# Kernel optimization log

Measured on AMD Instinct MI355X. Metric: run time of the kernel, lower is better.

The kernel has to match this reference:

```python
import jax, jax.numpy as jnp
import numpy as np

L2_IDX = np.array([0, 1, 2, 4, 24, 26, 35, 38])
S = 16    # n_scalar_features
H = 32    # hidden multiplicity
NL2 = 9   # number of 2e inputs (8 selected kernels + kernel sum)
B = 131072
NK = 40   # n_kernels


def _w3j_222():
    """Wigner 3j / CG tensor for 2e x 2e -> 2e in the real spherical-harmonic
    basis, Frobenius-normalized (e3nn convention up to an overall sign).
    Computed as the 1-D null space of the infinitesimal equivariance constraint."""
    l = 2
    mv = np.arange(-l, l + 1)
    Jp = np.zeros((5, 5), complex)
    for i, m in enumerate(mv[:-1]):
        Jp[i + 1, i] = np.sqrt(l * (l + 1) - m * (m + 1))
    Jm = Jp.conj().T
    Jx, Jy, Jz = (Jp + Jm) / 2, (Jp - Jm) / 2j, np.diag(mv).astype(complex)
    # complex -> real spherical harmonics change of basis
    Q = np.zeros((5, 5), complex)
    for m in mv:
        i = m + l
        if m < 0:
            Q[i, i] = 1j / np.sqrt(2)
            Q[i, l - m] = -1j * (-1.0) ** m / np.sqrt(2)
        elif m == 0:
            Q[i, i] = 1.0
        else:
            Q[i, l - m] = 1 / np.sqrt(2)
            Q[i, i] = (-1.0) ** m / np.sqrt(2)
    Gs = [np.real(-1j * Q @ J @ Q.conj().T) for J in (Jx, Jy, Jz)]  # real so(3) generators
    I5, I25 = np.eye(5), np.eye(25)
    M = np.concatenate([np.kron(G, I25) + np.kron(I5, np.kron(G, I5)) + np.kron(I25, G)
                        for G in Gs], axis=0)
    c = np.linalg.svd(M)[2][-1].reshape(5, 5, 5)
    c = c / np.linalg.norm(c)
    if c.flat[np.argmax(np.abs(c))] < 0:
        c = -c
    return c.astype(np.float32)


C222 = jnp.asarray(_w3j_222())
INV_SQRT5 = float(1.0 / np.sqrt(5.0))  # CG value for l,l->0 and 0,l->l paths


def setup_inputs() -> dict:
    key = jax.random.key(0)
    ks = jax.random.split(key, 10)
    return {
        "scalars": jax.random.normal(ks[0], (B, S), jnp.float32),
        "kernel_t2s": jax.random.normal(ks[1], (B, NK, 5), jnp.float32),
        "w000": jax.random.normal(ks[2], (S, S, H), jnp.float32),
        "w110": jax.random.normal(ks[3], (NL2, NL2, H), jnp.float32),
        "w011": jax.random.normal(ks[4], (S, NL2, H), jnp.float32),
        "w101": jax.random.normal(ks[5], (NL2, S, H), jnp.float32),
        "w111": jax.random.normal(ks[6], (NL2, NL2, H), jnp.float32),
        "v010": jax.random.normal(ks[7], (H, H), jnp.float32),
        "v100": jax.random.normal(ks[8], (H, H), jnp.float32),
        "v110": jax.random.normal(ks[9], (H, H), jnp.float32),
    }


def reference(scalars, kernel_t2s, w000, w110, w011, w101, w111, v010, v100, v110):
    s = scalars                                                  # (B, S)   0e inputs
    t = jnp.concatenate([kernel_t2s[:, L2_IDX, :],
                         kernel_t2s.sum(axis=1, keepdims=True)], axis=1)  # (B, 9, 5) 2e inputs

    # e3nn path-normalization coefficients (component / element defaults)
    c0 = (1.0 / (S * S + NL2 * NL2 * 5)) ** 0.5   # 0e out: fan-in S*S + 9*9*... -> S^2 + 81
    c0 = (1.0 / (S * S + 81)) ** 0.5
    c2 = (5.0 / (18 * S + 81)) ** 0.5             # 2e out: fan-in 9S + 9S + 81

    # ---- tp1(x, x): hidden = Hx0e + Hx2e ----
    h0 = c0 * (jnp.einsum('uvw,bu,bv->bw', w000, s, s)
               + INV_SQRT5 * jnp.einsum('uvw,bui,bvi->bw', w110, t, t))          # (B, H)
    u1 = jnp.einsum('bui,ijk->bujk', t, C222)                                    # (B,9,5,5)
    u2 = jnp.einsum('bujk,bvj->buvk', u1, t)                                     # (B,9,9,5)
    h2 = c2 * (INV_SQRT5 * jnp.einsum('uvw,bu,bvk->bwk', w011, s, t)
               + INV_SQRT5 * jnp.einsum('uvw,bui,bv->bwi', w101, t, s)
               + jnp.einsum('buvk,uvw->bwk', u2, w111))                          # (B, H, 5)

    # ---- tp2(h, h): 1x2e ----
    d = (5.0 / (3 * H * H)) ** 0.5
    a = jnp.einsum('uv,bvj->buj', v110, h2)       # (B, H, 5)
    b2 = jnp.einsum('bui,buj->bij', h2, a)        # (B, 5, 5)
    out = d * (INV_SQRT5 * (jnp.einsum('uv,bu,bvk->bk', v010, h0, h2)
                            + jnp.einsum('uv,buk,bv->bk', v100, h2, h0))
               + jnp.einsum('bij,ijk->bk', b2, C222))                            # (B, 5)
    return out
```

## Files before the change

### kernel.cpp

```cpp
#include <hip/hip_runtime.h>
#include <cmath>


#define DEVINL static __device__ __forceinline__

typedef _Float16 half2_t __attribute__((ext_vector_type(2)));
typedef _Float16 half8_t __attribute__((ext_vector_type(8)));
typedef float    f32x4_t __attribute__((ext_vector_type(4)));
union H8 { half8_t v; half2_t p[4]; };

#define FW0   0
#define FWC   6144
#define FMR   10752
#define FW111 11776
#define FV110 13824
#define SLABH 14848

__device__ __align__(16) _Float16 g_wsh[SLABH];

struct CPack { float v[32]; };

static constexpr int CIa[32] = {2,2,2,4,2,4,4,4, 2,0,0, 2,1,1, 2,3,3, 4,0,0, 4,1,1, 4,3,3, 0,0,1,1,3,3};
static constexpr int CJa[32] = {2,2,4,2,4,2,4,4, 0,2,0, 1,2,1, 3,2,3, 0,4,0, 1,4,1, 3,4,3, 1,3,0,3,0,1};
static constexpr int CKa[32] = {2,4,2,2,4,4,2,4, 0,0,2, 1,1,2, 3,3,2, 0,0,4, 1,1,4, 3,3,4, 3,1,3,0,1,0};

__host__ __device__ inline void tri_uv(int p, int n, int& u, int& v) {
  int base = 0;
  for (int x = 0; x < n; x++) {
    int c = n - x;
    if (p < base + c) { u = x; v = x + (p - base); return; }
    base += c;
  }
  u = n - 1; v = n - 1;
}

static double h_trE3(const double A[3][3], const double B[3][3], const double C[3][3]) {
  double t = 0.0;
  for (int r = 0; r < 3; r++)
    for (int c = 0; c < 3; c++) {
      double ab = 0.0;
      for (int m = 0; m < 3; m++) ab += A[r][m] * B[m][c];
      t += ab * C[c][r];
    }
  return t;
}
static void computeC(CPack& out) {
  const double s2i = 0.7071067811865475244, s6i = 0.4082482904638630164;
  double E[5][3][3] = {
    {{0, s2i, 0}, {s2i, 0, 0}, {0, 0, 0}},
    {{0, 0, 0}, {0, 0, s2i}, {0, s2i, 0}},
    {{-s6i, 0, 0}, {0, -s6i, 0}, {0, 0, 2.0 * s6i}},
    {{0, 0, s2i}, {0, 0, 0}, {s2i, 0, 0}},
    {{s2i, 0, 0}, {0, -s2i, 0}, {0, 0, 0}}
  };
  double T[125], nrm = 0.0;
  for (int f = 0; f < 125; f++) {
    int i = f / 25, j = (f / 5) % 5, k = f % 5;
    T[f] = h_trE3(E[i], E[j], E[k]) + h_trE3(E[i], E[k], E[j]);
    nrm += T[f] * T[f];
  }
  nrm = std::sqrt(nrm);
  int am = 0; double mx = std::fabs(T[0]);
  for (int q = 1; q < 125; q++) { double v = std::fabs(T[q]); if (v > mx) { mx = v; am = q; } }
  const double scale = ((T[am] < 0.0) ? 1.0 : -1.0) / nrm;
  for (int s = 0; s < 32; s++)
    out.v[s] = (float)(scale * T[(CIa[s] * 5 + CJa[s]) * 5 + CKa[s]]);
}

DEVINL float dot2f(half2_t a, half2_t b, float c) {
#if __has_builtin(__builtin_amdgcn_fdot2)
  return __builtin_amdgcn_fdot2(a, b, c, false);
#else
  return fmaf((float)a[0], (float)b[0], fmaf((float)a[1], (float)b[1], c));
#endif
}
DEVINL half2_t pk2(float a, float b) {
  auto r = __builtin_amdgcn_cvt_pkrtz(a, b);
  half2_t o;
  __builtin_memcpy(&o, &r, sizeof(o));
  return o;
}
DEVINL int h2i(half2_t h) { int i; __builtin_memcpy(&i, &h, 4); return i; }
DEVINL half2_t i2h(int i) { half2_t h; __builtin_memcpy(&h, &i, 4); return h; }
DEVINL f32x4_t mfma16(half8_t a, half8_t b, f32x4_t c) {
  return __builtin_amdgcn_mfma_f32_16x16x32_f16(a, b, c, 0, 0, 0);
}
DEVINL void store4h(_Float16* p, f32x4_t d) {
  int2 v;
  v.x = h2i(pk2(d[0], d[1]));
  v.y = h2i(pk2(d[2], d[3]));
  *(int2*)p = v;
}

DEVINL void bar_lds() {
  asm volatile("s_waitcnt lgkmcnt(0)" ::: "memory");
  __builtin_amdgcn_s_barrier();
  __builtin_amdgcn_sched_barrier(0);
}

__global__ void ech_setup(const float* __restrict__ w000, const float* __restrict__ w110,
                          const float* __restrict__ w011, const float* __restrict__ w101,
                          const float* __restrict__ w111, const float* __restrict__ v010,
                          const float* __restrict__ v100, const float* __restrict__ v110) {
  const float c0   = 1.0f / sqrtf(337.0f);
  const float inv5 = 0.44721359549995794f;
  const float c2   = sqrtf(5.0f / 369.0f);
  const float dm   = sqrtf(5.0f / 3072.0f) * inv5;
  int gid = blockIdx.x * blockDim.x + threadIdx.x;
  int gs  = gridDim.x * blockDim.x;

  for (int idx = gid; idx < 6144; idx += gs) {
    int j = idx & 7, L = (idx >> 3) & 63, tk = idx >> 9;
    int mt = tk / 6, ks = tk % 6;
    int w = mt * 16 + (L & 15);
    int p = ks * 32 + (L >> 4) * 8 + j;
    float x = 0.0f;
    if (p < 136) {
      int u, v; tri_uv(p, 16, u, v);
      x = c0 * (w000[(u * 16 + v) * 32 + w] + (u != v ? w000[(v * 16 + u) * 32 + w] : 0.0f));
    } else if (p < 181) {
      int u, v; tri_uv(p - 136, 9, u, v);
      x = c0 * inv5 * (w110[(u * 9 + v) * 32 + w] + (u != v ? w110[(v * 9 + u) * 32 + w] : 0.0f));
    }
    g_wsh[FW0 + idx] = (_Float16)x;
  }
  for (int idx = gid; idx < 4608; idx += gs) {
    int j = idx & 7, L = (idx >> 3) & 31, t = idx >> 8;
    int m = t * 16 + (L & 15);
    int w = m / 9, v = m % 9;
    int u = (L >> 4) * 8 + j;
    g_wsh[FWC + idx] =
        (_Float16)(c2 * inv5 * (w011[(u * 9 + v) * 32 + w] + w101[(v * 16 + u) * 32 + w]));
  }
  for (int idx = gid; idx < 1024; idx += gs) {
    int j = idx & 7, L = (idx >> 3) & 63, mt = idx >> 9;
    int w = mt * 16 + (L & 15);
    int u = (L >> 4) * 8 + j;
    g_wsh[FMR + idx] = (_Float16)(dm * (v010[u * 32 + w] + v100[w * 32 + u]));
  }
  for (int idx = gid; idx < 2048; idx += gs) {
    int j = idx & 7, L = (idx >> 3) & 63, t = idx >> 9;
    int mt = t >> 1, ks = t & 1;
    int w = mt * 16 + (L & 15);
    int p = ks * 32 + (L >> 4) * 8 + j;
    float x = 0.0f;
    if (p < 45) { int u, v; tri_uv(p, 9, u, v);
      x = c2 * (w111[(u * 9 + v) * 32 + w] + (u != v ? w111[(v * 9 + u) * 32 + w] : 0.0f)); }
    g_wsh[FW111 + idx] = (_Float16)x;
  }
  for (int idx = gid; idx < 1024; idx += gs) {
    int j = idx & 7, L = (idx >> 3) & 63, mt = idx >> 9;
    int u = mt * 16 + (L & 15);
    int v = (L >> 4) * 8 + j;
    g_wsh[FV110 + idx] = (_Float16)v110[u * 32 + v];
  }
}

#define ESZ 444
#define P5MT 272
#define P5K  544
__global__ void __launch_bounds__(512, 4)
ech_main(const float* __restrict__ sc, const float* __restrict__ t2s,
         float* __restrict__ out, int nGroups, CPack C) {
  __shared__ __align__(16) float scr[16 * ESZ];
  __shared__ __align__(16) _Float16 unionH[5280];
  __shared__ __align__(16) _Float16 cvvH[16 * 288];
  __shared__ __align__(16) _Float16 h0st[16 * 40];
  __shared__ __align__(16) _Float16 gst[16 * 40];
  __shared__ int pairs9[48];
  __shared__ int sspair[68];

  const int tid  = threadIdx.x;
  const int lane = tid & 31;
  const int sub  = tid >> 5;
  const int w    = lane;

  _Float16* p5H  = unionH;
  _Float16* h2Bb = unionH + 2720;

  if (tid < 45) { int u, v; tri_uv(tid, 9, u, v); pairs9[tid] = u | (v << 4); }
  if (tid < 68) {
    int u0, v0, u1, v1;
    tri_uv(2 * tid, 16, u0, v0);
    tri_uv(2 * tid + 1, 16, u1, v1);
    sspair[tid] = u0 | (v0 << 4) | (u1 << 8) | (v1 << 12);
  }

  constexpr int L2R[8] = {0, 1, 2, 4, 24, 26, 35, 38};

  float*     E    = scr + sub * ESZ;
  float*     Araw = E;
  _Float16*  qBe  = (_Float16*)E;
  float*     tb   = E + 200;
  _Float16*  sshh = (_Float16*)(E + 272);
  _Float16*  tthh = (_Float16*)(E + 340);
  _Float16*  thh  = (_Float16*)(E + 368);
  float*     sL   = E + 408;
  int*       spad = (int*)(E + 424);

  if (lane < 11)      tthh[45 + lane] = (_Float16)0.f;
  else if (lane < 16) thh[(lane - 11) * 16 + 9] = (_Float16)0.f;
  if (lane >= 24)     spad[lane - 16] = 0;

  float4 pf0 = {0.f, 0.f, 0.f, 0.f};
  float4 pf1 = {0.f, 0.f, 0.f, 0.f};
  float4 pfs = {0.f, 0.f, 0.f, 0.f};
  if (blockIdx.x < nGroups) {
    const int b0 = blockIdx.x * 16 + sub;
    const float4* src = (const float4*)(t2s + (size_t)b0 * 200);
    pf0 = src[lane];
    if (lane < 18) pf1 = src[lane + 32];
    if (lane < 4)  pfs = ((const float4*)(sc + (size_t)b0 * 16))[lane];
  }
  __syncthreads();

  for (int grp = blockIdx.x; grp < nGroups; grp += gridDim.x) {
    const int b = grp * 16 + sub;

    {
      float4* Av = (float4*)Araw;
      Av[lane] = pf0;
      if (lane < 18) Av[lane + 32] = pf1;
      if (lane < 4) ((float4*)sL)[lane] = pfs;
    }
    {
      const int gnext = grp + gridDim.x;
      if (gnext < nGroups) {
        const int bn = gnext * 16 + sub;
        const float4* srcn = (const float4*)(t2s + (size_t)bn * 200);
        pf0 = srcn[lane];
        if (lane < 18) pf1 = srcn[lane + 32];
        if (lane < 4)  pfs = ((const float4*)(sc + (size_t)bn * 16))[lane];
      }
    }
    if (lane < 8) spad[lane] = h2i(pk2(sL[2 * lane], sL[2 * lane + 1]));

    #pragma unroll
    for (int it = 0; it < 2; it++) {
      int idx = lane + 32 * it;
      if (idx < 40) {
        int r = idx / 5, c = idx % 5;
        float val = Araw[L2R[r] * 5 + c];
        tb[r * 8 + c] = val;
        thh[c * 16 + r] = (_Float16)val;
      }
    }
    {
      int l25 = lane % 25;
      int c2 = l25 / 5, j2 = l25 % 5;
      float acc = 0.f;
      #pragma unroll
      for (int rr = 0; rr < 8; rr++) acc += Araw[(j2 + 5 * rr) * 5 + c2];
      float tot = __shfl(acc, 5 * c2 + 0, 32) + __shfl(acc, 5 * c2 + 1, 32)
                + __shfl(acc, 5 * c2 + 2, 32) + __shfl(acc, 5 * c2 + 3, 32)
                + __shfl(acc, 5 * c2 + 4, 32);
      if (lane < 25 && j2 == 0) { tb[64 + c2] = tot; thh[c2 * 16 + 8] = (_Float16)tot; }
    }

    #pragma unroll
    for (int it = 0; it < 2; it++) {
      int idx = lane + 32 * it;
      if (idx < 45) {
        int pr = pairs9[idx];
        int pu = pr & 15, pv = pr >> 4;
        float4 u4 = *(const float4*)(tb + pu * 8); float u5 = tb[pu * 8 + 4];
        float4 v4 = *(const float4*)(tb + pv * 8); float v5 = tb[pv * 8 + 4];
        float tu[5] = {u4.x, u4.y, u4.z, u4.w, u5};
        float tv[5] = {v4.x, v4.y, v4.z, v4.w, v5};
        float tt = tu[0]*tv[0] + tu[1]*tv[1] + tu[2]*tv[2] + tu[3]*tv[3] + tu[4]*tv[4];
        tthh[idx] = (_Float16)tt;
        float qk[5] = {0, 0, 0, 0, 0};
        #pragma unroll
        for (int s = 0; s < 32; s++)
          qk[CKa[s]] = fmaf(C.v[s], tu[CIa[s]] * tv[CJa[s]], qk[CKa[s]]);
        #pragma unroll
        for (int k = 0; k < 5; k++) qBe[k * 64 + idx] = (_Float16)qk[k];
      } else {
        #pragma unroll
        for (int k = 0; k < 5; k++) qBe[k * 64 + idx] = (_Float16)0.f;
      }
    }

    #pragma unroll
    for (int ii = 0; ii < 3; ii++) {
      int slot = lane + 32 * ii;
      if (slot < 68) {
        int t = sspair[slot];
        int u0 = t & 15, v0 = (t >> 4) & 15, u1 = (t >> 8) & 15, v1 = (t >> 12) & 15;
        *(half2_t*)(sshh + 2 * slot) = pk2(sL[u0] * sL[v0], sL[u1] * sL[v1]);
      }
    }
    bar_lds();

    {
      const int wid = tid >> 6;
      const int L   = tid & 63;
      const int e2  = L & 15;
      const int q2  = L >> 4;
      const _Float16* scrH = (const _Float16*)scr;
      if (wid == 0) {
        f32x4_t a0 = {0.f, 0.f, 0.f, 0.f}, a1 = {0.f, 0.f, 0.f, 0.f};
        const _Float16* fw  = g_wsh + FW0 + (size_t)L * 8;
        const _Float16* ssb = scrH + e2 * (2 * ESZ) + 544;
        #pragma unroll
        for (int ks = 0; ks < 6; ks++) {
          half8_t bb = *(const half8_t*)(ssb + ks * 32 + q2 * 8);
          a0 = mfma16(*(const half8_t*)(fw + ks * 512), bb, a0);
          a1 = mfma16(*(const half8_t*)(fw + (6 + ks) * 512), bb, a1);
        }
        store4h(h0st + e2 * 40 + q2 * 4, a0);
        store4h(h0st + e2 * 40 + 16 + q2 * 4, a1);
      } else if (wid <= 2) {
        const _Float16* spb = scrH + e2 * (2 * ESZ) + 848;
        half8_t bb = *(const half8_t*)(spb + q2 * 8);
        const int t0 = (wid - 1) * 9;
        half8_t wz = {0, 0, 0, 0, 0, 0, 0, 0};
        #pragma unroll
        for (int t = 0; t < 9; t++) {
          half8_t wa = (q2 < 2)
              ? *(const half8_t*)(g_wsh + FWC + (t0 + t) * 256 + (size_t)L * 8) : wz;
          f32x4_t z4 = {0.f, 0.f, 0.f, 0.f};
          f32x4_t d = mfma16(wa, bb, z4);
          store4h(cvvH + e2 * 288 + (t0 + t) * 16 + q2 * 4, d);
        }
      } else {
        const int k = wid - 3;
        const _Float16* fw = g_wsh + FW111 + (size_t)L * 8;
        const _Float16* qb = scrH + e2 * (2 * ESZ) + k * 64;
        f32x4_t d0 = {0.f, 0.f, 0.f, 0.f}, d1 = {0.f, 0.f, 0.f, 0.f};
        #pragma unroll
        for (int ks = 0; ks < 2; ks++) {
          half8_t bb = *(const half8_t*)(qb + ks * 32 + q2 * 8);
          d0 = mfma16(*(const half8_t*)(fw + ks * 512), bb, d0);
          d1 = mfma16(*(const half8_t*)(fw + (2 + ks) * 512), bb, d1);
        }
        store4h(p5H + k * P5K + e2 * 16 + q2 * 4, d0);
        store4h(p5H + k * P5K + P5MT + e2 * 16 + q2 * 4, d1);
      }
    }
    bar_lds();

    float Cvv[9];
    #pragma unroll
    for (int v = 0; v < 9; v++) Cvv[v] = (float)cvvH[sub * 288 + w * 9 + v];
    half2_t cpk[5] = { pk2(Cvv[0], Cvv[1]), pk2(Cvv[2], Cvv[3]),
                       pk2(Cvv[4], Cvv[5]), pk2(Cvv[6], Cvv[7]), pk2(Cvv[8], 0.f) };
    float h2r[5];
    #pragma unroll
    for (int k = 0; k < 5; k++) {
      H8 d; d.v = *(const half8_t*)(thh + k * 16);
      half2_t d4 = *(const half2_t*)(thh + k * 16 + 8);
      float acc = dot2f(cpk[0], d.p[0], 0.f);
      acc = dot2f(cpk[1], d.p[1], acc);
      acc = dot2f(cpk[2], d.p[2], acc);
      acc = dot2f(cpk[3], d.p[3], acc);
      acc = dot2f(cpk[4], d4, acc);
      h2r[k] = acc + (float)p5H[k * P5K + (w >> 4) * P5MT + sub * 16 + (w & 15)];
    }
    #pragma unroll
    for (int k = 0; k < 5; k++) h2Bb[k * 512 + sub * 32 + w] = (_Float16)h2r[k];
    bar_lds();

    {
      const int wid = tid >> 6;
      const int L   = tid & 63;
      const int e2  = L & 15;
      const int q2  = L >> 4;
      if (wid < 5) {
        const int j = wid;
        const _Float16* fw = g_wsh + FV110 + (size_t)L * 8;
        half8_t bb = *(const half8_t*)(h2Bb + j * 512 + e2 * 32 + q2 * 8);
        f32x4_t z4 = {0.f, 0.f, 0.f, 0.f};
        f32x4_t d0 = mfma16(*(const half8_t*)(fw), bb, z4);
        f32x4_t d1 = mfma16(*(const half8_t*)(fw + 512), bb, z4);
        store4h(p5H + j * P5K + e2 * 16 + q2 * 4, d0);
        store4h(p5H + j * P5K + P5MT + e2 * 16 + q2 * 4, d1);
      } else if (wid == 5) {
        const _Float16* fw = g_wsh + FMR + (size_t)L * 8;
        half8_t hb = *(const half8_t*)(h0st + e2 * 40 + q2 * 8);
        f32x4_t z4 = {0.f, 0.f, 0.f, 0.f};
        f32x4_t g0 = mfma16(*(const half8_t*)(fw), hb, z4);
        f32x4_t g1 = mfma16(*(const half8_t*)(fw + 512), hb, z4);
        store4h(gst + e2 * 40 + q2 * 4, g0);
        store4h(gst + e2 * 40 + 16 + q2 * 4, g1);
      }
    }
    bar_lds();

    float a5[5];
    #pragma unroll
    for (int j = 0; j < 5; j++)
      a5[j] = (float)p5H[j * P5K + (w >> 4) * P5MT + sub * 16 + (w & 15)];
    float g = (float)gst[sub * 40 + w];

    float yv[5] = {0, 0, 0, 0, 0};
    #pragma unroll
    for (int s = 0; s < 32; s++)
      yv[CKa[s]] = fmaf(C.v[s], h2r[CIa[s]] * a5[CJa[s]], yv[CKa[s]]);

    const float DCONST = sqrtf(5.0f / 3072.0f);
    float z[5];
    #pragma unroll
    for (int k = 0; k < 5; k++) z[k] = fmaf(DCONST, yv[k], g * h2r[k]);

    half2_t z01 = pk2(z[0], z[1]);
    half2_t z23 = pk2(z[2], z[3]);
    float   z4r = z[4];
    #pragma unroll
    for (int st = 1; st <= 16; st <<= 1) {
      z01 = z01 + i2h(__shfl_xor(h2i(z01), st));
      z23 = z23 + i2h(__shfl_xor(h2i(z23), st));
      z4r += __shfl_xor(z4r, st);
    }
    if (lane < 5) {
      float val = (lane == 0) ? (float)z01[0]
                : (lane == 1) ? (float)z01[1]
                : (lane == 2) ? (float)z23[0]
                : (lane == 3) ? (float)z23[1] : z4r;
      out[(size_t)b * 5 + lane] = val;
    }
  }
}

extern "C" void kernel_launch(void* const* d_in, const int* in_sizes, int n_in,
                              void* d_out, int out_size, void* d_ws, size_t ws_size,
                              hipStream_t stream) {
  (void)n_in; (void)out_size; (void)d_ws; (void)ws_size;

  CPack C;
  computeC(C);

  ech_setup<<<64, 256, 0, stream>>>(
      (const float*)d_in[2], (const float*)d_in[3], (const float*)d_in[4],
      (const float*)d_in[5], (const float*)d_in[6], (const float*)d_in[7],
      (const float*)d_in[8], (const float*)d_in[9]);

  const int B = in_sizes[0] / 16;
  const int nGroups = B / 16;

  int grid = 768;
  if (grid > nGroups) grid = nGroups;

  ech_main<<<grid, 512, 0, stream>>>(
      (const float*)d_in[0], (const float*)d_in[1], (float*)d_out, nGroups, C);
}
```

Before: 272.3 us.

## Stage weights in LDS and replace final MFMA stage with per-wave dot products

Copies the packed fp16 weight slab from global memory into shared memory once per block and reads all MFMA weights from LDS. The last cross-wave MFMA stage (v110 and merged v010/v100 products) is replaced by per-lane packed dot2 loops over padded LDS rows, so two block barriers become a wave-local LDS fence. The grid is also reduced from 768 to 512 blocks. This adds LDS usage, which may lower occupancy, and moves that stage from matrix units to scalar dot instructions.

```diff
diff --git a/kernel.cpp b/kernel.cpp
--- a/kernel.cpp
+++ b/kernel.cpp
@@ -11,10 +11,10 @@
 
 #define FW0   0
 #define FWC   6144
-#define FMR   10752
-#define FW111 11776
-#define FV110 13824
-#define SLABH 14848
+#define FW111 10752
+#define PV110 12800
+#define PMR   13888
+#define SLABH 14976
 
 __device__ __align__(16) _Float16 g_wsh[SLABH];
 
@@ -97,6 +97,10 @@
   __builtin_amdgcn_s_barrier();
   __builtin_amdgcn_sched_barrier(0);
 }
+DEVINL void fence_lds_wave() {
+  asm volatile("s_waitcnt lgkmcnt(0)" ::: "memory");
+  __builtin_amdgcn_sched_barrier(0);
+}
 
 __global__ void ech_setup(const float* __restrict__ w000, const float* __restrict__ w110,
                           const float* __restrict__ w011, const float* __restrict__ w101,
@@ -132,12 +136,6 @@
     g_wsh[FWC + idx] =
         (_Float16)(c2 * inv5 * (w011[(u * 9 + v) * 32 + w] + w101[(v * 16 + u) * 32 + w]));
   }
-  for (int idx = gid; idx < 1024; idx += gs) {
-    int j = idx & 7, L = (idx >> 3) & 63, mt = idx >> 9;
-    int w = mt * 16 + (L & 15);
-    int u = (L >> 4) * 8 + j;
-    g_wsh[FMR + idx] = (_Float16)(dm * (v010[u * 32 + w] + v100[w * 32 + u]));
-  }
   for (int idx = gid; idx < 2048; idx += gs) {
     int j = idx & 7, L = (idx >> 3) & 63, t = idx >> 9;
     int mt = t >> 1, ks = t & 1;
@@ -149,10 +147,12 @@
     g_wsh[FW111 + idx] = (_Float16)x;
   }
   for (int idx = gid; idx < 1024; idx += gs) {
-    int j = idx & 7, L = (idx >> 3) & 63, mt = idx >> 9;
-    int u = mt * 16 + (L & 15);
-    int v = (L >> 4) * 8 + j;
-    g_wsh[FV110 + idx] = (_Float16)v110[u * 32 + v];
+    int u = idx >> 5, v = idx & 31;
+    g_wsh[PV110 + u * 34 + v] = (_Float16)v110[u * 32 + v];
+  }
+  for (int idx = gid; idx < 1024; idx += gs) {
+    int w = idx >> 5, u = idx & 31;
+    g_wsh[PMR + w * 34 + u] = (_Float16)(dm * (v010[u * 32 + w] + v100[w * 32 + u]));
   }
 }
 
@@ -162,11 +162,11 @@
 __global__ void __launch_bounds__(512, 4)
 ech_main(const float* __restrict__ sc, const float* __restrict__ t2s,
          float* __restrict__ out, int nGroups, CPack C) {
+  __shared__ __align__(16) _Float16 slabh[SLABH];
   __shared__ __align__(16) float scr[16 * ESZ];
   __shared__ __align__(16) _Float16 unionH[5280];
   __shared__ __align__(16) _Float16 cvvH[16 * 288];
   __shared__ __align__(16) _Float16 h0st[16 * 40];
-  __shared__ __align__(16) _Float16 gst[16 * 40];
   __shared__ int pairs9[48];
   __shared__ int sspair[68];
 
@@ -178,6 +178,8 @@
   _Float16* p5H  = unionH;
   _Float16* h2Bb = unionH + 2720;
 
+  for (int i = tid; i < SLABH / 8; i += 512)
+    ((float4*)slabh)[i] = ((const float4*)g_wsh)[i];
   if (tid < 45) { int u, v; tri_uv(tid, 9, u, v); pairs9[tid] = u | (v << 4); }
   if (tid < 68) {
     int u0, v0, u1, v1;
@@ -300,7 +302,7 @@
       const _Float16* scrH = (const _Float16*)scr;
       if (wid == 0) {
         f32x4_t a0 = {0.f, 0.f, 0.f, 0.f}, a1 = {0.f, 0.f, 0.f, 0.f};
-        const _Float16* fw  = g_wsh + FW0 + (size_t)L * 8;
+        const _Float16* fw  = slabh + FW0 + L * 8;
         const _Float16* ssb = scrH + e2 * (2 * ESZ) + 544;
         #pragma unroll
         for (int ks = 0; ks < 6; ks++) {
@@ -317,15 +319,14 @@
         half8_t wz = {0, 0, 0, 0, 0, 0, 0, 0};
         #pragma unroll
         for (int t = 0; t < 9; t++) {
-          half8_t wa = (q2 < 2)
-              ? *(const half8_t*)(g_wsh + FWC + (t0 + t) * 256 + (size_t)L * 8) : wz;
+          half8_t wa = (q2 < 2) ? *(const half8_t*)(slabh + FWC + (t0 + t) * 256 + L * 8) : wz;
           f32x4_t z4 = {0.f, 0.f, 0.f, 0.f};
           f32x4_t d = mfma16(wa, bb, z4);
           store4h(cvvH + e2 * 288 + (t0 + t) * 16 + q2 * 4, d);
         }
       } else {
         const int k = wid - 3;
-        const _Float16* fw = g_wsh + FW111 + (size_t)L * 8;
+        const _Float16* fw = slabh + FW111 + L * 8;
         const _Float16* qb = scrH + e2 * (2 * ESZ) + k * 64;
         f32x4_t d0 = {0.f, 0.f, 0.f, 0.f}, d1 = {0.f, 0.f, 0.f, 0.f};
         #pragma unroll
@@ -359,39 +360,31 @@
     }
     #pragma unroll
     for (int k = 0; k < 5; k++) h2Bb[k * 512 + sub * 32 + w] = (_Float16)h2r[k];
-    bar_lds();
-
+    fence_lds_wave();
+
+    float a5[5];
+    #pragma unroll
+    for (int j = 0; j < 5; j++) {
+      const _Float16* hb = h2Bb + j * 512 + sub * 32;
+      float acc = 0.f;
+      #pragma unroll
+      for (int vp = 0; vp < 16; vp++) {
+        half2_t wv = *(const half2_t*)(slabh + PV110 + w * 34 + 2 * vp);
+        half2_t hv = *(const half2_t*)(hb + 2 * vp);
+        acc = dot2f(wv, hv, acc);
+      }
+      a5[j] = acc;
+    }
+    float g = 0.f;
     {
-      const int wid = tid >> 6;
-      const int L   = tid & 63;
-      const int e2  = L & 15;
-      const int q2  = L >> 4;
-      if (wid < 5) {
-        const int j = wid;
-        const _Float16* fw = g_wsh + FV110 + (size_t)L * 8;
-        half8_t bb = *(const half8_t*)(h2Bb + j * 512 + e2 * 32 + q2 * 8);
-        f32x4_t z4 = {0.f, 0.f, 0.f, 0.f};
-        f32x4_t d0 = mfma16(*(const half8_t*)(fw), bb, z4);
-        f32x4_t d1 = mfma16(*(const half8_t*)(fw + 512), bb, z4);
-        store4h(p5H + j * P5K + e2 * 16 + q2 * 4, d0);
-        store4h(p5H + j * P5K + P5MT + e2 * 16 + q2 * 4, d1);
-      } else if (wid == 5) {
-        const _Float16* fw = g_wsh + FMR + (size_t)L * 8;
-        half8_t hb = *(const half8_t*)(h0st + e2 * 40 + q2 * 8);
-        f32x4_t z4 = {0.f, 0.f, 0.f, 0.f};
-        f32x4_t g0 = mfma16(*(const half8_t*)(fw), hb, z4);
-        f32x4_t g1 = mfma16(*(const half8_t*)(fw + 512), hb, z4);
-        store4h(gst + e2 * 40 + q2 * 4, g0);
-        store4h(gst + e2 * 40 + 16 + q2 * 4, g1);
-      }
-    }
-    bar_lds();
-
-    float a5[5];
-    #pragma unroll
-    for (int j = 0; j < 5; j++)
-      a5[j] = (float)p5H[j * P5K + (w >> 4) * P5MT + sub * 16 + (w & 15)];
-    float g = (float)gst[sub * 40 + w];
+      const _Float16* h0b = h0st + sub * 40;
+      #pragma unroll
+      for (int up = 0; up < 16; up++) {
+        half2_t wm = *(const half2_t*)(slabh + PMR + w * 34 + 2 * up);
+        half2_t hh = *(const half2_t*)(h0b + 2 * up);
+        g = dot2f(wm, hh, g);
+      }
+    }
 
     float yv[5] = {0, 0, 0, 0, 0};
     #pragma unroll
@@ -438,7 +431,7 @@
   const int B = in_sizes[0] / 16;
   const int nGroups = B / 16;
 
-  int grid = 768;
+  int grid = 512;
   if (grid > nGroups) grid = nGroups;
 
   ech_main<<<grid, 512, 0, stream>>>(
```

New measurement: 253.6 us. 6.9% less time.
